# Optimization experiments

Measured on AMD Instinct MI355X. Metric: run time of the kernel, lower is better.

## Reference

```python
import jax, jax.numpy as jnp
import numpy as np

FEATURE_DIM = 128  # user_aae.feature_dim == item_aae.feature_dim


def _encode(row, W1, b1, W2, b2):
    # row = [feature | x_rest]; original concatenates x and feature before the encoder MLP
    feat = row[:, :FEATURE_DIM]
    xr = row[:, FEATURE_DIM:]
    h = jax.nn.relu(jnp.concatenate([xr, feat], axis=-1) @ W1 + b1)
    return h @ W2 + b2  # [B, latent]


def setup_inputs() -> dict:
    key = jax.random.key(0)
    ks = jax.random.split(key, 12)
    B, NU, NI = 8192, 50000, 50000
    ROW, H, L = 2128, 512, 256  # feature_dim(128) + x_dim(2000)
    x = jnp.stack([
        jax.random.randint(ks[0], (B,), 0, NU),
        jax.random.randint(ks[1], (B,), 0, NI),
    ], axis=1).astype(jnp.int64)
    s1 = 1.0 / np.sqrt(ROW)
    s2 = 1.0 / np.sqrt(H)
    return {
        "x": x,
        "user_lookup": jax.random.normal(ks[2], (NU, ROW), jnp.float32),
        "item_lookup": jax.random.normal(ks[3], (NI, ROW), jnp.float32),
        "uW1": jax.random.normal(ks[4], (ROW, H), jnp.float32) * s1,
        "ub1": jnp.zeros((H,), jnp.float32),
        "uW2": jax.random.normal(ks[5], (H, L), jnp.float32) * s2,
        "ub2": jnp.zeros((L,), jnp.float32),
        "iW1": jax.random.normal(ks[6], (ROW, H), jnp.float32) * s1,
        "ib1": jnp.zeros((H,), jnp.float32),
        "iW2": jax.random.normal(ks[7], (H, L), jnp.float32) * s2,
        "ib2": jnp.zeros((L,), jnp.float32),
    }


def reference(x, user_lookup, item_lookup, uW1, ub1, uW2, ub2, iW1, ib1, iW2, ib2):
    user_row = user_lookup[x[:, 0]]  # [B, ROW]
    item_row = item_lookup[x[:, 1]]  # [B, ROW]
    u = _encode(user_row, uW1, ub1, uW2, ub2)  # [B, L]
    v = _encode(item_row, iW1, ib1, iW2, ib2)  # [B, L]
    # diag(u @ v.T) == rowwise dot product (identical math, no B x B matrix)
    diag = jnp.sum(u * v, axis=-1)
    return diag[:, None]  # [B, 1]
```

## Files before the change

kernel.cpp:

```cpp
#include <hip/hip_runtime.h>
#include <stdint.h>

typedef __attribute__((ext_vector_type(8))) short bf16x8;
typedef __attribute__((ext_vector_type(4))) float f32x4;

#define MFMA16(a, b, c) __builtin_amdgcn_mfma_f32_16x16x32_bf16((a), (b), (c), 0, 0, 0)

static __device__ __forceinline__ unsigned f2bf(float f) {
  union { float f; unsigned u; } cv;
  cv.f = f;
  return (cv.u + 0x7fffu + ((cv.u >> 16) & 1u)) >> 16;
}

#define BATCH 8192
#define ROWD  2128
#define HID   512
#define LATD  256
#define KC1   272
#define NT1   68
#define HSL_TW (BATCH * HID)

__global__ __launch_bounds__(256) void ASAECF_tcast(
    const float* __restrict__ in0, const float* __restrict__ in1,
    unsigned short* __restrict__ out, int N, int lgN, int Kin, int KC, int perm)
{
  const float* __restrict__ in = blockIdx.z ? in1 : in0;
  unsigned short* __restrict__ o = out + (size_t)blockIdx.z * KC * N * 8;
  const int s = blockIdx.x * 256 + threadIdx.x;
  const int kc = s >> lgN, n = s & (N - 1);
  unsigned short v[8];
#pragma unroll
  for (int e = 0; e < 8; ++e) {
    const int k = kc * 8 + e;
    float f = 0.0f;
    if (k < Kin) {
      const int src = perm ? (k < 128 ? k + 2000 : k - 128) : k;
      f = in[(size_t)src * N + n];
    }
    v[e] = (unsigned short)f2bf(f);
  }
  *(uint4*)(o + (size_t)s * 8) = *(const uint4*)v;
}

__global__ __launch_bounds__(1024) void ASAECF_gemm1(
    const int* __restrict__ x,
    const float* __restrict__ ulook, const float* __restrict__ ilook,
    const unsigned short* __restrict__ w1s,
    const float* __restrict__ ub1, const float* __restrict__ ib1,
    unsigned short* __restrict__ hsl)
{
  const int bid   = blockIdx.x;
  const int xcd   = bid & 7;
  const int idx   = bid >> 3;
  const int tower = xcd >> 2;
  const int nh    = idx & 1;
  const int mb    = (xcd & 3) * 16 + (idx >> 1);

  const float* __restrict__ look = tower ? ilook : ulook;
  const unsigned short* __restrict__ w1 = w1s + (size_t)tower * KC1 * HID * 8;
  const float* __restrict__ b1 = tower ? ib1 : ub1;
  unsigned short* __restrict__ hout = hsl + (size_t)tower * HSL_TW;

  __shared__ unsigned short Ab[2][128 * 40];

  const int tid  = threadIdx.x;
  const int lane = tid & 63, wid = tid >> 6;
  const int wm   = wid >> 2, wn = wid & 3;
  const int fr   = lane & 15, fq = lane >> 4;
  const int row0 = mb * 128;

  const int ar = tid >> 3, ak = (tid & 7) * 4;
  const long long arow = (long long)x[(row0 + ar) * 2 + tower] * ROWD + ak;

  int boff[4];
#pragma unroll
  for (int n = 0; n < 4; ++n)
    boff[n] = (fq * 512 + nh * 256 + wn * 64 + n * 16 + fr) * 8;

  auto loadA = [&](int tt) -> f32x4 {
    f32x4 v = {0.0f, 0.0f, 0.0f, 0.0f};
    if (tt * 32 + ak <= ROWD - 4)
      v = *(const f32x4*)(look + arow + tt * 32);
    return v;
  };
  auto writeA = [&](int buf, f32x4 v) {
    uint2 p;
    p.x = f2bf(v[0]) | (f2bf(v[1]) << 16);
    p.y = f2bf(v[2]) | (f2bf(v[3]) << 16);
    *(uint2*)&Ab[buf][ar * 40 + ak] = p;
  };

  f32x4 acc[2][4] = {};
  bf16x8 bgc[4], bgn[4];
  f32x4 rA0, rA1;

  writeA(0, loadA(0));
  rA0 = loadA(1);
  rA1 = loadA(2);
#pragma unroll
  for (int n = 0; n < 4; ++n) bgc[n] = *(const bf16x8*)(w1 + boff[n]);

#pragma unroll 2
  for (int t = 0; t < NT1; ++t) {
    __syncthreads();
    const int cu = t & 1;

    const unsigned short* bpn = w1 + (size_t)(t + 1) * (4 * 512 * 8);
#pragma unroll
    for (int n = 0; n < 4; ++n) bgn[n] = *(const bf16x8*)(bpn + boff[n]);

    bf16x8 af[2];
#pragma unroll
    for (int m = 0; m < 2; ++m)
      af[m] = *(const bf16x8*)&Ab[cu][(wm * 32 + m * 16 + fr) * 40 + fq * 8];
#pragma unroll
    for (int n = 0; n < 4; ++n)
#pragma unroll
      for (int m = 0; m < 2; ++m)
        acc[m][n] = MFMA16(af[m], bgc[n], acc[m][n]);

    if (cu == 0) { writeA(1, rA0); rA0 = loadA(t + 3); }
    else         { writeA(0, rA1); rA1 = loadA(t + 3); }

#pragma unroll
    for (int n = 0; n < 4; ++n) bgc[n] = bgn[n];
  }

#pragma unroll
  for (int n = 0; n < 4; ++n) {
    const int col = nh * 256 + wn * 64 + n * 16 + fr;
    const int kc = col >> 3, e = col & 7;
    const float bb = b1[col];
#pragma unroll
    for (int m = 0; m < 2; ++m)
#pragma unroll
      for (int i = 0; i < 4; ++i) {
        const int rowib = wm * 32 + m * 16 + fq * 4 + i;
        const int chunk = mb * 2 + (rowib >> 6);
        const int row = rowib & 63;
        const float v = fmaxf(acc[m][n][i] + bb, 0.0f);
        hout[(((size_t)chunk * 64 + kc) * 64 + row) * 8 + e] = (unsigned short)f2bf(v);
      }
  }
}

__global__ __launch_bounds__(512, 2) void ASAECF_gemm2dot(
    const unsigned short* __restrict__ hsl,
    const unsigned short* __restrict__ w2s,
    const float* __restrict__ ub2, const float* __restrict__ ib2,
    float* __restrict__ out)
{
  const int tid  = threadIdx.x;
  const int lane = tid & 63, wid = tid >> 6;
  const int fr   = lane & 15, fq = lane >> 4;
  const int rb   = blockIdx.x;
  const int row0 = rb * 32;

  const unsigned short* __restrict__ hu = hsl;
  const unsigned short* __restrict__ hv = hsl + (size_t)HSL_TW;
  const size_t abase = ((size_t)(rb >> 1) * 64) * 64 * 8;
  const int lrow0 = (rb & 1) * 32;

  f32x4 au[2][2] = {}, av[2][2] = {};

#pragma unroll
  for (int t = 0; t < 8; ++t) {
#pragma unroll
    for (int s = 0; s < 2; ++s) {
      const int kc = t * 8 + s * 4 + fq;
      bf16x8 a_u[2], a_v[2], b_u[2], b_v[2];
#pragma unroll
      for (int m = 0; m < 2; ++m) {
        const size_t off = abase + ((size_t)kc * 64 + lrow0 + m * 16 + fr) * 8;
        a_u[m] = *(const bf16x8*)(hu + off);
        a_v[m] = *(const bf16x8*)(hv + off);
      }
#pragma unroll
      for (int n = 0; n < 2; ++n) {
        const int col = wid * 32 + n * 16 + fr;
        const size_t offb = ((size_t)kc * 256 + col) * 8;
        b_u[n] = *(const bf16x8*)(w2s + offb);
        b_v[n] = *(const bf16x8*)(w2s + (size_t)64 * 256 * 8 + offb);
      }
#pragma unroll
      for (int m = 0; m < 2; ++m)
#pragma unroll
        for (int n = 0; n < 2; ++n) {
          au[m][n] = MFMA16(a_u[m], b_u[n], au[m][n]);
          av[m][n] = MFMA16(a_v[m], b_v[n], av[m][n]);
        }
    }
  }

  __shared__ float red[8][32];
  float bu[2], bv[2];
#pragma unroll
  for (int n = 0; n < 2; ++n) {
    const int col = wid * 32 + n * 16 + fr;
    bu[n] = ub2[col];
    bv[n] = ib2[col];
  }
#pragma unroll
  for (int m = 0; m < 2; ++m)
#pragma unroll
    for (int i = 0; i < 4; ++i) {
      float p = 0.0f;
#pragma unroll
      for (int n = 0; n < 2; ++n)
        p += (au[m][n][i] + bu[n]) * (av[m][n][i] + bv[n]);
      p += __shfl_xor(p, 1, 64);
      p += __shfl_xor(p, 2, 64);
      p += __shfl_xor(p, 4, 64);
      p += __shfl_xor(p, 8, 64);
      if (fr == 0) red[wid][m * 16 + fq * 4 + i] = p;
    }
  __syncthreads();
  if (tid < 32) {
    float s = 0.0f;
#pragma unroll
    for (int w = 0; w < 8; ++w) s += red[w][tid];
    out[row0 + tid] = s;
  }
}

extern "C" void kernel_launch(void* const* d_in, const int* in_sizes, int n_in,
                              void* d_out, int out_size, void* d_ws, size_t ws_size,
                              hipStream_t stream) {
  (void)in_sizes; (void)n_in; (void)out_size; (void)ws_size;
  const int*   x     = (const int*)d_in[0];
  const float* ulook = (const float*)d_in[1];
  const float* ilook = (const float*)d_in[2];
  const float* uW1   = (const float*)d_in[3];
  const float* ub1   = (const float*)d_in[4];
  const float* uW2   = (const float*)d_in[5];
  const float* ub2   = (const float*)d_in[6];
  const float* iW1   = (const float*)d_in[7];
  const float* ib1   = (const float*)d_in[8];
  const float* iW2   = (const float*)d_in[9];
  const float* ib2   = (const float*)d_in[10];
  float* out = (float*)d_out;

  char* ws = (char*)d_ws;
  unsigned short* w1s = (unsigned short*)(ws);
  unsigned short* w2s = (unsigned short*)(ws + 4456448);
  unsigned short* hsl = (unsigned short*)(ws + 4980736);

  ASAECF_tcast<<<dim3(544, 1, 2), 256, 0, stream>>>(uW1, iW1, w1s, 512, 9, ROWD, KC1, 1);
  ASAECF_tcast<<<dim3(64, 1, 2),  256, 0, stream>>>(uW2, iW2, w2s, 256, 8, HID, 64, 0);
  ASAECF_gemm1<<<dim3(256), 1024, 0, stream>>>(x, ulook, ilook, w1s, ub1, ib1, hsl);
  ASAECF_gemm2dot<<<dim3(256), 512, 0, stream>>>(hsl, w2s, ub2, ib2, out);
}
```

Measured before the change: 91.17 us.

## Restructure gemm1 with LDS-staged W1 via direct global-to-LDS loads and larger warp tiles

Rewrites the first GEMM to use 512 threads, each wave computing a 64x64 tile, with K steps of 64 instead of 32. W1 tiles are now staged into dynamically allocated, double-buffered LDS through global_load_lds instead of each wave reading them into registers from global memory. The epilogue goes through LDS so hidden activations are written as coalesced 16-byte stores. The intent is to cut redundant W1 global traffic, halve the barrier count and improve store efficiency. In exchange it uses more LDS and more accumulator registers per thread, which may lower occupancy.

After: 93.35 us. 2.4% more time.

```diff
diff --git a/kernel.cpp b/kernel.cpp
--- a/kernel.cpp
+++ b/kernel.cpp
@@ -5,6 +5,12 @@
 typedef __attribute__((ext_vector_type(4))) float f32x4;
 
 #define MFMA16(a, b, c) __builtin_amdgcn_mfma_f32_16x16x32_bf16((a), (b), (c), 0, 0, 0)
+
+__device__ __forceinline__ void gload_lds16(const void* g, void* l) {
+  __builtin_amdgcn_global_load_lds((const __attribute__((address_space(1))) void*)g,
+                                   (__attribute__((address_space(3))) void*)l,
+                                   16, 0, 0);
+}
 
 static __device__ __forceinline__ unsigned f2bf(float f) {
   union { float f; unsigned u; } cv;
@@ -17,8 +23,13 @@
 #define HID   512
 #define LATD  256
 #define KC1   272
-#define NT1   68
+#define NT2   34
 #define HSL_TW (BATCH * HID)
+
+#define A_BUF 9216
+#define B_OFF (2 * A_BUF)
+#define B_BUF 16384
+#define LDS_BYTES ((B_OFF + 2 * B_BUF) * 2)
 
 __global__ __launch_bounds__(256) void ASAECF_tcast(
     const float* __restrict__ in0, const float* __restrict__ in1,
@@ -42,13 +53,15 @@
   *(uint4*)(o + (size_t)s * 8) = *(const uint4*)v;
 }
 
-__global__ __launch_bounds__(1024) void ASAECF_gemm1(
+__global__ __launch_bounds__(512) void ASAECF_gemm1(
     const int* __restrict__ x,
     const float* __restrict__ ulook, const float* __restrict__ ilook,
     const unsigned short* __restrict__ w1s,
     const float* __restrict__ ub1, const float* __restrict__ ib1,
     unsigned short* __restrict__ hsl)
 {
+  extern __shared__ unsigned short LDS[];
+
   const int bid   = blockIdx.x;
   const int xcd   = bid & 7;
   const int idx   = bid >> 3;
@@ -61,86 +74,105 @@
   const float* __restrict__ b1 = tower ? ib1 : ub1;
   unsigned short* __restrict__ hout = hsl + (size_t)tower * HSL_TW;
 
-  __shared__ unsigned short Ab[2][128 * 40];
-
   const int tid  = threadIdx.x;
   const int lane = tid & 63, wid = tid >> 6;
   const int wm   = wid >> 2, wn = wid & 3;
   const int fr   = lane & 15, fq = lane >> 4;
   const int row0 = mb * 128;
 
-  const int ar = tid >> 3, ak = (tid & 7) * 4;
-  const long long arow = (long long)x[(row0 + ar) * 2 + tower] * ROWD + ak;
-
-  int boff[4];
-#pragma unroll
-  for (int n = 0; n < 4; ++n)
-    boff[n] = (fq * 512 + nh * 256 + wn * 64 + n * 16 + fr) * 8;
-
-  auto loadA = [&](int tt) -> f32x4 {
-    f32x4 v = {0.0f, 0.0f, 0.0f, 0.0f};
-    if (tt * 32 + ak <= ROWD - 4)
-      v = *(const f32x4*)(look + arow + tt * 32);
-    return v;
+  const int ar  = tid >> 2;
+  const int q16 = (tid & 3) * 16;
+  const long long abase = (long long)x[(row0 + ar) * 2 + tower] * ROWD;
+
+  f32x4 rA[4];
+  auto loadA = [&](int t) {
+    const int kb = t * 64 + q16;
+#pragma unroll
+    for (int i = 0; i < 4; ++i) {
+      rA[i] = f32x4{0.0f, 0.0f, 0.0f, 0.0f};
+      if (kb + i * 4 + 4 <= ROWD)
+        rA[i] = *(const f32x4*)(look + abase + kb + i * 4);
+    }
   };
-  auto writeA = [&](int buf, f32x4 v) {
-    uint2 p;
-    p.x = f2bf(v[0]) | (f2bf(v[1]) << 16);
-    p.y = f2bf(v[2]) | (f2bf(v[3]) << 16);
-    *(uint2*)&Ab[buf][ar * 40 + ak] = p;
+  auto writeA = [&](int buf) {
+    unsigned short v[16];
+#pragma unroll
+    for (int i = 0; i < 4; ++i)
+#pragma unroll
+      for (int e = 0; e < 4; ++e)
+        v[i * 4 + e] = (unsigned short)f2bf(rA[i][e]);
+    unsigned short* d = &LDS[buf * A_BUF + ar * 72 + q16];
+    *(bf16x8*)d = *(const bf16x8*)v;
+    *(bf16x8*)(d + 8) = *(const bf16x8*)(v + 8);
   };
-
-  f32x4 acc[2][4] = {};
-  bf16x8 bgc[4], bgn[4];
-  f32x4 rA0, rA1;
-
-  writeA(0, loadA(0));
-  rA0 = loadA(1);
-  rA1 = loadA(2);
-#pragma unroll
-  for (int n = 0; n < 4; ++n) bgc[n] = *(const bf16x8*)(w1 + boff[n]);
-
-#pragma unroll 2
-  for (int t = 0; t < NT1; ++t) {
+  auto stageB = [&](int t, int buf) {
+    unsigned short* bd = &LDS[B_OFF + buf * B_BUF + wid * 256 * 8];
+    const unsigned short* gs = w1 + ((size_t)(t * 8 + wid) * 512 + nh * 256) * 8;
+#pragma unroll
+    for (int cg = 0; cg < 4; ++cg)
+      gload_lds16(gs + (cg * 64 + lane) * 8, bd + cg * 64 * 8);
+  };
+
+  f32x4 acc[4][4] = {};
+
+  loadA(0);
+  stageB(0, 0);
+  writeA(0);
+  __syncthreads();
+
+  int buf = 0;
+  for (int t = 0; t < NT2; ++t) {
+    const bool pre = (t + 1 < NT2);
+    if (pre) { stageB(t + 1, buf ^ 1); loadA(t + 1); }
+
+#pragma unroll
+    for (int ks = 0; ks < 2; ++ks) {
+      bf16x8 af[4], bg[4];
+#pragma unroll
+      for (int m = 0; m < 4; ++m)
+        af[m] = *(const bf16x8*)&LDS[buf * A_BUF + (wm * 64 + m * 16 + fr) * 72 + ks * 32 + fq * 8];
+#pragma unroll
+      for (int n = 0; n < 4; ++n)
+        bg[n] = *(const bf16x8*)&LDS[B_OFF + buf * B_BUF + (((ks * 4 + fq) * 256) + wn * 64 + n * 16 + fr) * 8];
+#pragma unroll
+      for (int n = 0; n < 4; ++n)
+#pragma unroll
+        for (int m = 0; m < 4; ++m)
+          acc[m][n] = MFMA16(af[m], bg[n], acc[m][n]);
+    }
+
+    if (pre) writeA(buf ^ 1);
     __syncthreads();
-    const int cu = t & 1;
-
-    const unsigned short* bpn = w1 + (size_t)(t + 1) * (4 * 512 * 8);
-#pragma unroll
-    for (int n = 0; n < 4; ++n) bgn[n] = *(const bf16x8*)(bpn + boff[n]);
-
-    bf16x8 af[2];
-#pragma unroll
-    for (int m = 0; m < 2; ++m)
-      af[m] = *(const bf16x8*)&Ab[cu][(wm * 32 + m * 16 + fr) * 40 + fq * 8];
-#pragma unroll
-    for (int n = 0; n < 4; ++n)
-#pragma unroll
-      for (int m = 0; m < 2; ++m)
-        acc[m][n] = MFMA16(af[m], bgc[n], acc[m][n]);
-
-    if (cu == 0) { writeA(1, rA0); rA0 = loadA(t + 3); }
-    else         { writeA(0, rA1); rA1 = loadA(t + 3); }
-
-#pragma unroll
-    for (int n = 0; n < 4; ++n) bgc[n] = bgn[n];
-  }
-
+    buf ^= 1;
+  }
+
+  unsigned short* W = &LDS[wid * 64 * 72];
 #pragma unroll
   for (int n = 0; n < 4; ++n) {
-    const int col = nh * 256 + wn * 64 + n * 16 + fr;
-    const int kc = col >> 3, e = col & 7;
-    const float bb = b1[col];
-#pragma unroll
-    for (int m = 0; m < 2; ++m)
+    const int col_l = n * 16 + fr;
+    const float bb = b1[nh * 256 + wn * 64 + col_l];
+#pragma unroll
+    for (int m = 0; m < 4; ++m)
 #pragma unroll
       for (int i = 0; i < 4; ++i) {
-        const int rowib = wm * 32 + m * 16 + fq * 4 + i;
-        const int chunk = mb * 2 + (rowib >> 6);
-        const int row = rowib & 63;
+        const int row_l = m * 16 + fq * 4 + i;
         const float v = fmaxf(acc[m][n][i] + bb, 0.0f);
-        hout[(((size_t)chunk * 64 + kc) * 64 + row) * 8 + e] = (unsigned short)f2bf(v);
+        W[row_l * 72 + col_l] = (unsigned short)f2bf(v);
       }
+  }
+  __syncthreads();
+  {
+    const int g  = lane >> 3;
+    const int ri = lane & 7;
+    const int kc = (nh * 256 + wn * 64 + g * 8) >> 3;
+    const int chunk = mb * 2 + wm;
+    unsigned short* hb = hout + ((size_t)(chunk * 64 + kc) * 64) * 8;
+#pragma unroll
+    for (int rr = 0; rr < 8; ++rr) {
+      const int row_l = rr * 8 + ri;
+      bf16x8 val = *(const bf16x8*)&W[row_l * 72 + g * 8];
+      *(bf16x8*)&hb[row_l * 8] = val;
+    }
   }
 }
 
@@ -247,6 +279,6 @@
 
   ASAECF_tcast<<<dim3(544, 1, 2), 256, 0, stream>>>(uW1, iW1, w1s, 512, 9, ROWD, KC1, 1);
   ASAECF_tcast<<<dim3(64, 1, 2),  256, 0, stream>>>(uW2, iW2, w2s, 256, 8, HID, 64, 0);
-  ASAECF_gemm1<<<dim3(256), 1024, 0, stream>>>(x, ulook, ilook, w1s, ub1, ib1, hsl);
+  ASAECF_gemm1<<<dim3(256), 512, LDS_BYTES, stream>>>(x, ulook, ilook, w1s, ub1, ib1, hsl);
   ASAECF_gemm2dot<<<dim3(256), 512, 0, stream>>>(hsl, w2s, ub2, ib2, out);
 }
```

## Halve gemm1 block to 8 waves with full-row tiles; merge weight cast launches

Applied to the files above, without the earlier changes.

The first GEMM now runs with 512 threads, and each wave computes all 128 rows against a 32-column slice instead of a 32x64 sub-tile. This cuts the per-wave B-fragment loads and raises MFMA work per LDS A-fragment read, at the cost of more accumulator registers (16 f32x4) and more LDS reads of A per wave. Each thread now gathers 8 floats per step instead of 4. The two weight-cast kernels are also merged into one launch using blockIdx.y, removing one kernel launch.

New measurement: 77.75 us, median of 2. 1.17x faster.

```diff
diff --git a/kernel.cpp b/kernel.cpp
--- a/kernel.cpp
+++ b/kernel.cpp
@@ -20,13 +20,10 @@
 #define NT1   68
 #define HSL_TW (BATCH * HID)
 
-__global__ __launch_bounds__(256) void ASAECF_tcast(
-    const float* __restrict__ in0, const float* __restrict__ in1,
-    unsigned short* __restrict__ out, int N, int lgN, int Kin, int KC, int perm)
-{
-  const float* __restrict__ in = blockIdx.z ? in1 : in0;
-  unsigned short* __restrict__ o = out + (size_t)blockIdx.z * KC * N * 8;
-  const int s = blockIdx.x * 256 + threadIdx.x;
+__device__ __forceinline__ void tcast_body(
+    const float* __restrict__ in, unsigned short* __restrict__ o,
+    int s, int N, int lgN, int Kin, int perm)
+{
   const int kc = s >> lgN, n = s & (N - 1);
   unsigned short v[8];
 #pragma unroll
@@ -42,7 +39,24 @@
   *(uint4*)(o + (size_t)s * 8) = *(const uint4*)v;
 }
 
-__global__ __launch_bounds__(1024) void ASAECF_gemm1(
+__global__ __launch_bounds__(256) void ASAECF_tcast(
+    const float* __restrict__ uW1, const float* __restrict__ iW1,
+    const float* __restrict__ uW2, const float* __restrict__ iW2,
+    unsigned short* __restrict__ w1s, unsigned short* __restrict__ w2s)
+{
+  const int tower = blockIdx.z;
+  const int s = blockIdx.x * 256 + threadIdx.x;
+  if (blockIdx.y == 0) {
+    tcast_body(tower ? iW1 : uW1, w1s + (size_t)tower * KC1 * HID * 8,
+               s, HID, 9, ROWD, 1);
+  } else {
+    if (blockIdx.x >= 64) return;
+    tcast_body(tower ? iW2 : uW2, w2s + (size_t)tower * 64 * LATD * 8,
+               s, LATD, 8, HID, 0);
+  }
+}
+
+__global__ __launch_bounds__(512) void ASAECF_gemm1(
     const int* __restrict__ x,
     const float* __restrict__ ulook, const float* __restrict__ ilook,
     const unsigned short* __restrict__ w1s,
@@ -65,40 +79,47 @@
 
   const int tid  = threadIdx.x;
   const int lane = tid & 63, wid = tid >> 6;
-  const int wm   = wid >> 2, wn = wid & 3;
   const int fr   = lane & 15, fq = lane >> 4;
   const int row0 = mb * 128;
 
-  const int ar = tid >> 3, ak = (tid & 7) * 4;
+  const int ar = tid >> 2, ak = (tid & 3) * 8;
   const long long arow = (long long)x[(row0 + ar) * 2 + tower] * ROWD + ak;
 
-  int boff[4];
-#pragma unroll
-  for (int n = 0; n < 4; ++n)
-    boff[n] = (fq * 512 + nh * 256 + wn * 64 + n * 16 + fr) * 8;
-
-  auto loadA = [&](int tt) -> f32x4 {
-    f32x4 v = {0.0f, 0.0f, 0.0f, 0.0f};
-    if (tt * 32 + ak <= ROWD - 4)
-      v = *(const f32x4*)(look + arow + tt * 32);
+  int boff[2];
+#pragma unroll
+  for (int n = 0; n < 2; ++n)
+    boff[n] = (fq * 512 + nh * 256 + wid * 32 + n * 16 + fr) * 8;
+
+  struct A8 { f32x4 a, b; };
+  auto loadA = [&](int tt) -> A8 {
+    A8 v;
+    v.a = f32x4{0.0f, 0.0f, 0.0f, 0.0f};
+    v.b = f32x4{0.0f, 0.0f, 0.0f, 0.0f};
+    if (tt * 32 + ak + 8 <= ROWD) {
+      v.a = *(const f32x4*)(look + arow + tt * 32);
+      v.b = *(const f32x4*)(look + arow + tt * 32 + 4);
+    }
     return v;
   };
-  auto writeA = [&](int buf, f32x4 v) {
-    uint2 p;
-    p.x = f2bf(v[0]) | (f2bf(v[1]) << 16);
-    p.y = f2bf(v[2]) | (f2bf(v[3]) << 16);
+  auto writeA = [&](int buf, A8 v) {
+    uint2 p, q;
+    p.x = f2bf(v.a[0]) | (f2bf(v.a[1]) << 16);
+    p.y = f2bf(v.a[2]) | (f2bf(v.a[3]) << 16);
+    q.x = f2bf(v.b[0]) | (f2bf(v.b[1]) << 16);
+    q.y = f2bf(v.b[2]) | (f2bf(v.b[3]) << 16);
     *(uint2*)&Ab[buf][ar * 40 + ak] = p;
+    *(uint2*)&Ab[buf][ar * 40 + ak + 4] = q;
   };
 
-  f32x4 acc[2][4] = {};
-  bf16x8 bgc[4], bgn[4];
-  f32x4 rA0, rA1;
+  f32x4 acc[8][2] = {};
+  bf16x8 bgc[2], bgn[2];
+  A8 rA0, rA1;
 
   writeA(0, loadA(0));
   rA0 = loadA(1);
   rA1 = loadA(2);
 #pragma unroll
-  for (int n = 0; n < 4; ++n) bgc[n] = *(const bf16x8*)(w1 + boff[n]);
+  for (int n = 0; n < 2; ++n) bgc[n] = *(const bf16x8*)(w1 + boff[n]);
 
 #pragma unroll 2
   for (int t = 0; t < NT1; ++t) {
@@ -107,35 +128,35 @@
 
     const unsigned short* bpn = w1 + (size_t)(t + 1) * (4 * 512 * 8);
 #pragma unroll
-    for (int n = 0; n < 4; ++n) bgn[n] = *(const bf16x8*)(bpn + boff[n]);
-
-    bf16x8 af[2];
-#pragma unroll
-    for (int m = 0; m < 2; ++m)
-      af[m] = *(const bf16x8*)&Ab[cu][(wm * 32 + m * 16 + fr) * 40 + fq * 8];
-#pragma unroll
-    for (int n = 0; n < 4; ++n)
-#pragma unroll
-      for (int m = 0; m < 2; ++m)
+    for (int n = 0; n < 2; ++n) bgn[n] = *(const bf16x8*)(bpn + boff[n]);
+
+    bf16x8 af[8];
+#pragma unroll
+    for (int m = 0; m < 8; ++m)
+      af[m] = *(const bf16x8*)&Ab[cu][(m * 16 + fr) * 40 + fq * 8];
+#pragma unroll
+    for (int n = 0; n < 2; ++n)
+#pragma unroll
+      for (int m = 0; m < 8; ++m)
         acc[m][n] = MFMA16(af[m], bgc[n], acc[m][n]);
 
     if (cu == 0) { writeA(1, rA0); rA0 = loadA(t + 3); }
     else         { writeA(0, rA1); rA1 = loadA(t + 3); }
 
 #pragma unroll
-    for (int n = 0; n < 4; ++n) bgc[n] = bgn[n];
-  }
-
-#pragma unroll
-  for (int n = 0; n < 4; ++n) {
-    const int col = nh * 256 + wn * 64 + n * 16 + fr;
+    for (int n = 0; n < 2; ++n) bgc[n] = bgn[n];
+  }
+
+#pragma unroll
+  for (int n = 0; n < 2; ++n) {
+    const int col = nh * 256 + wid * 32 + n * 16 + fr;
     const int kc = col >> 3, e = col & 7;
     const float bb = b1[col];
 #pragma unroll
-    for (int m = 0; m < 2; ++m)
+    for (int m = 0; m < 8; ++m)
 #pragma unroll
       for (int i = 0; i < 4; ++i) {
-        const int rowib = wm * 32 + m * 16 + fq * 4 + i;
+        const int rowib = m * 16 + fq * 4 + i;
         const int chunk = mb * 2 + (rowib >> 6);
         const int row = rowib & 63;
         const float v = fmaxf(acc[m][n][i] + bb, 0.0f);
@@ -245,8 +266,7 @@
   unsigned short* w2s = (unsigned short*)(ws + 4456448);
   unsigned short* hsl = (unsigned short*)(ws + 4980736);
 
-  ASAECF_tcast<<<dim3(544, 1, 2), 256, 0, stream>>>(uW1, iW1, w1s, 512, 9, ROWD, KC1, 1);
-  ASAECF_tcast<<<dim3(64, 1, 2),  256, 0, stream>>>(uW2, iW2, w2s, 256, 8, HID, 64, 0);
-  ASAECF_gemm1<<<dim3(256), 1024, 0, stream>>>(x, ulook, ilook, w1s, ub1, ib1, hsl);
+  ASAECF_tcast<<<dim3(544, 2, 2), 256, 0, stream>>>(uW1, iW1, uW2, iW2, w1s, w2s);
+  ASAECF_gemm1<<<dim3(256), 512, 0, stream>>>(x, ulook, ilook, w1s, ub1, ib1, hsl);
   ASAECF_gemm2dot<<<dim3(256), 512, 0, stream>>>(hsl, w2s, ub2, ib2, out);
 }
```
